# Optimization experiments

Measured on AMD Instinct MI355X. Metric: run time of the kernel, lower is better.

The kernel has to match this reference:

```python
import math
import jax, jax.numpy as jnp
import numpy as np

D_MODEL = 1024
N_HEADS = 16
HEAD_DIM = D_MODEL // N_HEADS
B, S = 4, 1024


def setup_inputs() -> dict:
    key = jax.random.key(0)
    ks = jax.random.split(key, 20)
    def lin(kw, kb):
        # torch nn.Linear: weight [out, in], y = x @ W.T + b
        w = jax.random.normal(kw, (D_MODEL, D_MODEL), jnp.float32) * 0.02
        b = jax.random.normal(kb, (D_MODEL,), jnp.float32) * 0.02
        return w, b
    inp = {
        'global_feat': jax.random.normal(ks[0], (B, S, D_MODEL), jnp.float32),
        'local_feat': jax.random.normal(ks[1], (B, S, D_MODEL), jnp.float32),
        'text_feat': jax.random.normal(ks[2], (B, S, D_MODEL), jnp.float32),
    }
    names = ['glb_q', 'glb_k', 'glb_v', 'plb_q', 'plb_k', 'plb_v', 'dense']
    for i, n in enumerate(names):
        w, b = lin(ks[3 + 2 * i], ks[4 + 2 * i])
        inp[n + '_w'] = w
        inp[n + '_b'] = b
    return inp


def _heads(x):
    # [B,S,D] -> [B,H,S,dh]
    b, s, _ = x.shape
    return x.reshape(b, s, N_HEADS, HEAD_DIM).transpose(0, 2, 1, 3)


def _merge(x):
    # [B,H,S,dh] -> [B,S,D]
    b, h, s, d = x.shape
    return x.transpose(0, 2, 1, 3).reshape(b, s, h * d)


def reference(global_feat, local_feat, text_feat,
              glb_q_w, glb_q_b, glb_k_w, glb_k_b, glb_v_w, glb_v_b,
              plb_q_w, plb_q_b, plb_k_w, plb_k_b, plb_v_w, plb_v_b,
              dense_w, dense_b):
    scale = 1.0 / math.sqrt(HEAD_DIM)
    gq = _heads(global_feat @ glb_q_w.T + glb_q_b)
    gk = _heads(local_feat @ glb_k_w.T + glb_k_b)
    gv = _heads(local_feat @ glb_v_w.T + glb_v_b)
    pq = _heads(local_feat @ plb_q_w.T + plb_q_b)
    pk = _heads(text_feat @ plb_k_w.T + plb_k_b)
    pv = _heads(text_feat @ plb_v_w.T + plb_v_b)

    glb_probs = jax.nn.softmax(jnp.einsum('bhqd,bhkd->bhqk', gq, gk) * scale, axis=-1)
    plb_probs = jax.nn.softmax(jnp.einsum('bhqd,bhkd->bhqk', pq, pk) * scale, axis=-1)

    # bridge: matmul of the two probability matrices (dropout disabled / eval)
    plb_enhanced = jnp.einsum('bhql,bhlt->bhqt', glb_probs, plb_probs)

    glb_ctx = jnp.einsum('bhqk,bhkd->bhqd', glb_probs, gv)
    plb_ctx = jnp.einsum('bhqt,bhtd->bhqd', plb_enhanced, pv)

    last = _merge(glb_ctx) + _merge(plb_ctx)
    return last @ dense_w.T + dense_b
```

## Files before the change

kernel.cpp:

```cpp
#include <hip/hip_runtime.h>


#define DEVI static __device__ __forceinline__

typedef __attribute__((ext_vector_type(4))) float f32x4;
typedef __attribute__((ext_vector_type(8))) __bf16 bf16x8;
typedef __attribute__((ext_vector_type(8))) short s16x8;
typedef __attribute__((ext_vector_type(4))) short s16x4;

constexpr int S = 1024, D = 1024, NH = 16, DH = 64, NB = 4;
constexpr int M = NB * S;
constexpr int KD = 1024;
constexpr int ND = 1024;
constexpr float QSCALE = 0.18033688011112042f;

DEVI short f2bf(float f) {
  unsigned u = __builtin_bit_cast(unsigned, f);
  u += 0x7FFFu + ((u >> 16) & 1u);
  return (short)(u >> 16);
}

DEVI f32x4 mfma_bf16(s16x8 a, s16x8 b, f32x4 c) {
  return __builtin_amdgcn_mfma_f32_16x16x32_bf16(
      __builtin_bit_cast(bf16x8, a), __builtin_bit_cast(bf16x8, b), c, 0, 0, 0);
}

DEVI void gll16(const void* g, void* l) {
  __builtin_amdgcn_global_load_lds(
      (const __attribute__((address_space(1))) unsigned*)g,
      (__attribute__((address_space(3))) unsigned*)l, 16, 0, 0);
}

struct Ptrs3 { const float* p0; const float* p1; const float* p2; };
struct Ptrs7 { const float* p[7]; };

__global__ __launch_bounds__(256) void cast_inputs(Ptrs3 in, short* __restrict__ out) {
  int b = blockIdx.x;
  int which = b >> 12;
  const float* src = which == 0 ? in.p0 : (which == 1 ? in.p1 : in.p2);
  size_t local = ((size_t)(b & 4095) * 256 + threadIdx.x) * 4;
  f32x4 v = *(const f32x4*)(src + local);
  s16x4 o = { f2bf(v[0]), f2bf(v[1]), f2bf(v[2]), f2bf(v[3]) };
  *(s16x4*)(out + (size_t)which * ((size_t)M * KD) + local) = o;
}

__global__ __launch_bounds__(256) void cast_weights(Ptrs7 in, short* __restrict__ out) {
  int b = blockIdx.x;
  int which = b >> 10;
  size_t local = ((size_t)(b & 1023) * 256 + threadIdx.x) * 4;
  f32x4 v = *(const f32x4*)(in.p[which] + local);
  s16x4 o = { f2bf(v[0]), f2bf(v[1]), f2bf(v[2]), f2bf(v[3]) };
  *(s16x4*)(out + (size_t)which * 1048576 + local) = o;
}

DEVI void stage_ab(const short* A, const short* Bw, int rowBase, int colBase, int k0,
                   short* Asb, short* Bsb, int tid) {
  const int cr = tid >> 2;
  const int cb = (tid & 3) * 16;
  const int sw = ((cr >> 1) & 3) << 4;
  gll16((const char*)(A + (size_t)(rowBase + cr) * KD + k0) + (cb ^ sw), Asb + tid * 8);
  gll16((const char*)(A + (size_t)(rowBase + 64 + cr) * KD + k0) + (cb ^ sw), Asb + (tid + 256) * 8);
  gll16((const char*)(Bw + (size_t)(colBase + cr) * KD + k0) + (cb ^ sw), Bsb + tid * 8);
  gll16((const char*)(Bw + (size_t)(colBase + 64 + cr) * KD + k0) + (cb ^ sw), Bsb + (tid + 256) * 8);
}

struct GemmBatch {
  const short* A[6];
  const float* bias[6];
  void* out[6];
};

__global__ __launch_bounds__(256) void gemm_proj(GemmBatch gb, const short* __restrict__ W) {
  __shared__ short As[2][128 * 32];
  __shared__ short Bs[2][128 * 32];
  const int wg = (blockIdx.x & 7) * 192 + (blockIdx.x >> 3);
  const int z = wg >> 8;
  const int rem = wg & 255;
  const int rowBase = (rem >> 3) * 128, colBase = (rem & 7) * 128;

  const short* A = gb.A[z];
  const short* Bw = W + (size_t)z * ((size_t)KD * ND);
  const float* bias = gb.bias[z];
  const float scale = (z == 0 || z == 3) ? QSCALE : 1.0f;
  const int f32out = (z == 2);

  const int tid = threadIdx.x;
  const int lane = tid & 63, wave = tid >> 6;
  const int wr = wave >> 1, wc = wave & 1;
  const int l15 = lane & 15, lg = lane >> 4;
  const int rs = ((l15 >> 1) & 3) << 3;

  stage_ab(A, Bw, rowBase, colBase, 0, As[0], Bs[0], tid);
  __syncthreads();

  f32x4 acc[4][4] = {};
  int buf = 0;
  for (int k0 = 0; k0 < KD; k0 += 32) {
    if (k0 + 32 < KD)
      stage_ab(A, Bw, rowBase, colBase, k0 + 32, As[buf ^ 1], Bs[buf ^ 1], tid);
    s16x8 af[4], bf[4];
#pragma unroll
    for (int m = 0; m < 4; m++)
      af[m] = *(const s16x8*)(As[buf] + (wr * 64 + m * 16 + l15) * 32 + ((lg * 8) ^ rs));
#pragma unroll
    for (int n = 0; n < 4; n++)
      bf[n] = *(const s16x8*)(Bs[buf] + (wc * 64 + n * 16 + l15) * 32 + ((lg * 8) ^ rs));
#pragma unroll
    for (int m = 0; m < 4; m++)
#pragma unroll
      for (int n = 0; n < 4; n++)
        acc[m][n] = mfma_bf16(af[m], bf[n], acc[m][n]);
    __syncthreads();
    buf ^= 1;
  }

  const int r0 = lg * 4;
#pragma unroll
  for (int m = 0; m < 4; m++)
#pragma unroll
    for (int n = 0; n < 4; n++)
#pragma unroll
      for (int i = 0; i < 4; i++) {
        int row = rowBase + wr * 64 + m * 16 + r0 + i;
        int col = colBase + wc * 64 + n * 16 + l15;
        float v = (acc[m][n][i] + bias[col]) * scale;
        size_t idx = (((size_t)(row >> 10) * NH + (col >> 6)) * S + (row & (S - 1))) * DH + (col & (DH - 1));
        if (f32out) ((float*)gb.out[z])[idx] = v;
        else        ((short*)gb.out[z])[idx] = f2bf(v);
      }
}

__global__ __launch_bounds__(256) void gemm_dense(const short* __restrict__ A,
                                                  const short* __restrict__ Bw,
                                                  const float* __restrict__ bias,
                                                  float* __restrict__ outp) {
  __shared__ short As[2][128 * 32];
  __shared__ short Bs[2][128 * 32];
  const int wg = (blockIdx.x & 7) * 32 + (blockIdx.x >> 3);
  const int rowBase = (wg >> 3) * 128, colBase = (wg & 7) * 128;

  const int tid = threadIdx.x;
  const int lane = tid & 63, wave = tid >> 6;
  const int wr = wave >> 1, wc = wave & 1;
  const int l15 = lane & 15, lg = lane >> 4;
  const int rs = ((l15 >> 1) & 3) << 3;

  stage_ab(A, Bw, rowBase, colBase, 0, As[0], Bs[0], tid);
  __syncthreads();

  f32x4 acc[4][4] = {};
  int buf = 0;
  for (int k0 = 0; k0 < KD; k0 += 32) {
    if (k0 + 32 < KD)
      stage_ab(A, Bw, rowBase, colBase, k0 + 32, As[buf ^ 1], Bs[buf ^ 1], tid);
    s16x8 af[4], bf[4];
#pragma unroll
    for (int m = 0; m < 4; m++)
      af[m] = *(const s16x8*)(As[buf] + (wr * 64 + m * 16 + l15) * 32 + ((lg * 8) ^ rs));
#pragma unroll
    for (int n = 0; n < 4; n++)
      bf[n] = *(const s16x8*)(Bs[buf] + (wc * 64 + n * 16 + l15) * 32 + ((lg * 8) ^ rs));
#pragma unroll
    for (int m = 0; m < 4; m++)
#pragma unroll
      for (int n = 0; n < 4; n++)
        acc[m][n] = mfma_bf16(af[m], bf[n], acc[m][n]);
    __syncthreads();
    buf ^= 1;
  }

  const int r0 = lg * 4;
#pragma unroll
  for (int m = 0; m < 4; m++)
#pragma unroll
    for (int n = 0; n < 4; n++)
#pragma unroll
      for (int i = 0; i < 4; i++) {
        int row = rowBase + wr * 64 + m * 16 + r0 + i;
        int col = colBase + wc * 64 + n * 16 + l15;
        outp[(size_t)row * ND + col] = acc[m][n][i] + bias[col];
      }
}

__global__ __launch_bounds__(256) void transpose_bf16(const short* __restrict__ in,
                                                      short* __restrict__ out) {
  __shared__ short t[64 * 65];
  const int bh = blockIdx.y, s0 = blockIdx.x * 64;
  const int tid = threadIdx.x;
#pragma unroll
  for (int j = 0; j < 16; j++) {
    int e = j * 256 + tid;
    int s = e >> 6, d = e & 63;
    t[d * 65 + s] = in[((size_t)bh * S + s0 + s) * DH + d];
  }
  __syncthreads();
#pragma unroll
  for (int j = 0; j < 16; j++) {
    int e = j * 256 + tid;
    int d = e >> 6, s = e & 63;
    out[((size_t)bh * DH + d) * S + s0 + s] = t[d * 65 + s];
  }
}

__global__ __launch_bounds__(256) void vprime_t(const float* __restrict__ gv,
                                                const float* __restrict__ pa,
                                                short* __restrict__ out) {
  __shared__ short t[64 * 65];
  const int bh = blockIdx.y, s0 = blockIdx.x * 64;
  const int tid = threadIdx.x;
#pragma unroll
  for (int j = 0; j < 16; j++) {
    int e = j * 256 + tid;
    int s = e >> 6, d = e & 63;
    size_t idx = ((size_t)bh * S + s0 + s) * DH + d;
    t[d * 65 + s] = f2bf(gv[idx] + pa[idx]);
  }
  __syncthreads();
#pragma unroll
  for (int j = 0; j < 16; j++) {
    int e = j * 256 + tid;
    int d = e >> 6, s = e & 63;
    out[((size_t)bh * DH + d) * S + s0 + s] = t[d * 65 + s];
  }
}

DEVI void stage_kv(const short* kb, const short* vb, int kt,
                   short* KT, short* VTs, int tid) {
  const int r0 = tid >> 3, cb = (tid & 7) * 16;
  const int r1 = r0 + 32;
  const int sw0 = (r0 & 7) << 4;
  gll16((const char*)kb + (size_t)(kt + r0) * 128 + (cb ^ sw0), KT + tid * 8);
  gll16((const char*)kb + (size_t)(kt + r1) * 128 + (cb ^ sw0), KT + (tid + 256) * 8);
  gll16((const char*)vb + (size_t)r0 * 2048 + (size_t)kt * 2 + (cb ^ sw0), VTs + tid * 8);
  gll16((const char*)vb + (size_t)r1 * 2048 + (size_t)kt * 2 + (cb ^ sw0), VTs + (tid + 256) * 8);
}

template <int OUTMODE>
__global__ __launch_bounds__(256, 4) void attn64(const short* __restrict__ Q,
                                                 const short* __restrict__ Km,
                                                 const short* __restrict__ Vt,
                                                 void* __restrict__ outp) {
  __shared__ short KT[2][64 * 64];
  __shared__ short VTs[2][64 * 64];
  __shared__ short Pl[4][1024];
  const int tid = threadIdx.x, lane = tid & 63, wave = tid >> 6;
  const int l15 = lane & 15, lg = lane >> 4;
  const int w = blockIdx.x;
  const int sw = (w & 7) * 128 + (w >> 3);
  const int bh = sw >> 4;
  const int q0 = (sw & 15) * 64 + wave * 16;

  const short* qp = Q + ((size_t)bh * S + q0 + l15) * DH + lg * 8;
  s16x8 qf0 = *(const s16x8*)qp;
  s16x8 qf1 = *(const s16x8*)(qp + 32);

  const short* kb = Km + (size_t)bh * S * DH;
  const short* vb = Vt + (size_t)bh * DH * S;
  short* myP = Pl[wave];
  const int rsz = (l15 & 7) << 3;
  const s16x8 ones = { 0x3F80, 0x3F80, 0x3F80, 0x3F80, 0x3F80, 0x3F80, 0x3F80, 0x3F80 };

  stage_kv(kb, vb, 0, KT[0], VTs[0], tid);
  __syncthreads();

  f32x4 acc[4] = {};
  f32x4 accS = {};

  for (int kt = 0; kt < S; kt += 64) {
    const int cur = (kt >> 6) & 1;
    if (kt + 64 < S) stage_kv(kb, vb, kt + 64, KT[cur ^ 1], VTs[cur ^ 1], tid);

    f32x4 sf[4];
#pragma unroll
    for (int n = 0; n < 4; n++) {
      const short* kr = KT[cur] + (n * 16 + l15) * 64;
      s16x8 k0 = *(const s16x8*)(kr + ((lg * 8) ^ rsz));
      s16x8 k1 = *(const s16x8*)(kr + ((32 + lg * 8) ^ rsz));
      sf[n] = mfma_bf16(qf0, k0, f32x4{});
      sf[n] = mfma_bf16(qf1, k1, sf[n]);
    }

    f32x4 p[4];
#pragma unroll
    for (int n = 0; n < 4; n++)
#pragma unroll
      for (int i = 0; i < 4; i++) p[n][i] = exp2f(sf[n][i]);

#pragma unroll
    for (int n = 0; n < 4; n++)
#pragma unroll
      for (int i = 0; i < 4; i++) {
        int row = lg * 4 + i;
        myP[row * 64 + ((n * 16 + l15) ^ ((row & 7) << 3))] = f2bf(p[n][i]);
      }
    asm volatile("s_waitcnt lgkmcnt(0)" ::: "memory");
    s16x8 pa0 = *(const s16x8*)(myP + l15 * 64 + ((lg * 8) ^ rsz));
    s16x8 pa1 = *(const s16x8*)(myP + l15 * 64 + ((32 + lg * 8) ^ rsz));

    accS = mfma_bf16(pa0, ones, accS);
    accS = mfma_bf16(pa1, ones, accS);

#pragma unroll
    for (int n = 0; n < 4; n++) {
      const short* vr = VTs[cur] + (n * 16 + l15) * 64;
      s16x8 v0 = *(const s16x8*)(vr + ((lg * 8) ^ rsz));
      s16x8 v1 = *(const s16x8*)(vr + ((32 + lg * 8) ^ rsz));
      acc[n] = mfma_bf16(pa0, v0, acc[n]);
      acc[n] = mfma_bf16(pa1, v1, acc[n]);
    }

    __syncthreads();
  }

  float inv[4];
#pragma unroll
  for (int i = 0; i < 4; i++) inv[i] = 1.f / accS[i];
#pragma unroll
  for (int n = 0; n < 4; n++)
#pragma unroll
    for (int i = 0; i < 4; i++) {
      int qq = q0 + lg * 4 + i;
      int dc = n * 16 + l15;
      float v = acc[n][i] * inv[i];
      if (OUTMODE == 0)
        ((float*)outp)[((size_t)bh * S + qq) * DH + dc] = v;
      else
        ((short*)outp)[((size_t)(bh >> 4) * S + qq) * D + (bh & 15) * DH + dc] = f2bf(v);
    }
}

extern "C" void kernel_launch(void* const* d_in, const int* in_sizes, int n_in,
                              void* d_out, int out_size, void* d_ws, size_t ws_size,
                              hipStream_t stream) {
  const float* xg = (const float*)d_in[0];
  const float* xl = (const float*)d_in[1];
  const float* xt = (const float*)d_in[2];
  const float* wf[7]; const float* bf_[7];
  for (int i = 0; i < 7; i++) { wf[i] = (const float*)d_in[3 + 2 * i]; bf_[i] = (const float*)d_in[4 + 2 * i]; }

  char* ws = (char*)d_ws;
  size_t off = 0;
  auto alloc = [&](size_t bytes) { void* p = ws + off; off += (bytes + 255) & ~(size_t)255; return p; };
  short* x16   = (short*)alloc((size_t)3 * M * KD * 2);
  short* w16   = (short*)alloc((size_t)7 * KD * ND * 2);
  short* gq16  = (short*)alloc((size_t)M * D * 2);
  short* gk16  = (short*)alloc((size_t)M * D * 2);
  float* gv32  = (float*)alloc((size_t)M * D * 4);
  short* pq16  = (short*)alloc((size_t)M * D * 2);
  short* pk16  = (short*)alloc((size_t)M * D * 2);
  short* pv16  = (short*)alloc((size_t)M * D * 2);
  short* pvt16 = (short*)alloc((size_t)M * D * 2);
  float* plb32 = (float*)alloc((size_t)M * D * 4);
  short* vpt16 = (short*)alloc((size_t)M * D * 2);
  short* last16= (short*)alloc((size_t)M * D * 2);
  (void)ws_size; (void)in_sizes; (void)n_in; (void)out_size;

  short* xg16 = x16;
  short* xl16 = x16 + (size_t)M * KD;
  short* xt16 = x16 + (size_t)2 * M * KD;

  Ptrs3 p3{xg, xl, xt};
  cast_inputs<<<3 * 4096, 256, 0, stream>>>(p3, x16);
  Ptrs7 p7; for (int i = 0; i < 7; i++) p7.p[i] = wf[i];
  cast_weights<<<7 * 1024, 256, 0, stream>>>(p7, w16);

  GemmBatch gb;
  gb.A[0] = xg16; gb.A[1] = xl16; gb.A[2] = xl16; gb.A[3] = xl16; gb.A[4] = xt16; gb.A[5] = xt16;
  for (int i = 0; i < 6; i++) gb.bias[i] = bf_[i];
  gb.out[0] = gq16; gb.out[1] = gk16; gb.out[2] = gv32;
  gb.out[3] = pq16; gb.out[4] = pk16; gb.out[5] = pv16;
  gemm_proj<<<1536, 256, 0, stream>>>(gb, w16);

  dim3 gt(S / 64, NB * NH);
  transpose_bf16<<<gt, 256, 0, stream>>>(pv16, pvt16);
  attn64<0><<<1024, 256, 0, stream>>>(pq16, pk16, pvt16, plb32);
  vprime_t<<<gt, 256, 0, stream>>>(gv32, plb32, vpt16);
  attn64<1><<<1024, 256, 0, stream>>>(gq16, gk16, vpt16, last16);

  gemm_dense<<<256, 256, 0, stream>>>(last16, w16 + (size_t)6 * 1048576, bf_[6], (float*)d_out);
}
```

Baseline: 326.1 us.

## Fuse V-prime add/transpose into attention epilogue and widen attention to 128 queries

The first attention kernel now adds the bf16 global V projection in its epilogue and writes the transposed bf16 V' directly, which removes the vprime_t kernel and the fp32 plb/gv intermediates. The gv projection is stored as bf16 instead of fp32, and each wave now handles 32 query rows (128 per block), so every K/V tile staged in LDS is reused across twice as many queries. s_setprio and sched_barrier hints are added around the MFMA sections. In exchange, gv carries bf16 rounding error, register use goes up, the block count halves and occupancy drops to 2 blocks per SM, and the transposed epilogue stores are strided.

```diff
diff --git a/kernel.cpp b/kernel.cpp
--- a/kernel.cpp
+++ b/kernel.cpp
@@ -29,6 +29,11 @@
   __builtin_amdgcn_global_load_lds(
       (const __attribute__((address_space(1))) unsigned*)g,
       (__attribute__((address_space(3))) unsigned*)l, 16, 0, 0);
+}
+
+DEVI float bf2f(short s) {
+  unsigned u = (unsigned)(unsigned short)s << 16;
+  return __builtin_bit_cast(float, u);
 }
 
 struct Ptrs3 { const float* p0; const float* p1; const float* p2; };
@@ -67,7 +72,7 @@
 struct GemmBatch {
   const short* A[6];
   const float* bias[6];
-  void* out[6];
+  short* out[6];
 };
 
 __global__ __launch_bounds__(256) void gemm_proj(GemmBatch gb, const short* __restrict__ W) {
@@ -82,7 +87,6 @@
   const short* Bw = W + (size_t)z * ((size_t)KD * ND);
   const float* bias = gb.bias[z];
   const float scale = (z == 0 || z == 3) ? QSCALE : 1.0f;
-  const int f32out = (z == 2);
 
   const int tid = threadIdx.x;
   const int lane = tid & 63, wave = tid >> 6;
@@ -125,8 +129,7 @@
         int col = colBase + wc * 64 + n * 16 + l15;
         float v = (acc[m][n][i] + bias[col]) * scale;
         size_t idx = (((size_t)(row >> 10) * NH + (col >> 6)) * S + (row & (S - 1))) * DH + (col & (DH - 1));
-        if (f32out) ((float*)gb.out[z])[idx] = v;
-        else        ((short*)gb.out[z])[idx] = f2bf(v);
+        gb.out[z][idx] = f2bf(v);
       }
 }
 
@@ -192,28 +195,6 @@
     int e = j * 256 + tid;
     int s = e >> 6, d = e & 63;
     t[d * 65 + s] = in[((size_t)bh * S + s0 + s) * DH + d];
-  }
-  __syncthreads();
-#pragma unroll
-  for (int j = 0; j < 16; j++) {
-    int e = j * 256 + tid;
-    int d = e >> 6, s = e & 63;
-    out[((size_t)bh * DH + d) * S + s0 + s] = t[d * 65 + s];
-  }
-}
-
-__global__ __launch_bounds__(256) void vprime_t(const float* __restrict__ gv,
-                                                const float* __restrict__ pa,
-                                                short* __restrict__ out) {
-  __shared__ short t[64 * 65];
-  const int bh = blockIdx.y, s0 = blockIdx.x * 64;
-  const int tid = threadIdx.x;
-#pragma unroll
-  for (int j = 0; j < 16; j++) {
-    int e = j * 256 + tid;
-    int s = e >> 6, d = e & 63;
-    size_t idx = ((size_t)bh * S + s0 + s) * DH + d;
-    t[d * 65 + s] = f2bf(gv[idx] + pa[idx]);
   }
   __syncthreads();
 #pragma unroll
@@ -236,23 +217,28 @@
 }
 
 template <int OUTMODE>
-__global__ __launch_bounds__(256, 4) void attn64(const short* __restrict__ Q,
-                                                 const short* __restrict__ Km,
-                                                 const short* __restrict__ Vt,
-                                                 void* __restrict__ outp) {
+__global__ __launch_bounds__(256, 2) void attn128(const short* __restrict__ Q,
+                                                  const short* __restrict__ Km,
+                                                  const short* __restrict__ Vt,
+                                                  const short* __restrict__ gv,
+                                                  void* __restrict__ outp) {
   __shared__ short KT[2][64 * 64];
   __shared__ short VTs[2][64 * 64];
-  __shared__ short Pl[4][1024];
+  __shared__ short Pl[4][32 * 64];
   const int tid = threadIdx.x, lane = tid & 63, wave = tid >> 6;
   const int l15 = lane & 15, lg = lane >> 4;
   const int w = blockIdx.x;
-  const int sw = (w & 7) * 128 + (w >> 3);
-  const int bh = sw >> 4;
-  const int q0 = (sw & 15) * 64 + wave * 16;
-
-  const short* qp = Q + ((size_t)bh * S + q0 + l15) * DH + lg * 8;
-  s16x8 qf0 = *(const s16x8*)qp;
-  s16x8 qf1 = *(const s16x8*)(qp + 32);
+  const int sw = (w & 7) * 64 + (w >> 3);
+  const int bh = sw >> 3;
+  const int q0 = (sw & 7) * 128 + wave * 32;
+
+  s16x8 qf[2][2];
+#pragma unroll
+  for (int q = 0; q < 2; q++) {
+    const short* qp = Q + ((size_t)bh * S + q0 + q * 16 + l15) * DH + lg * 8;
+    qf[q][0] = *(const s16x8*)qp;
+    qf[q][1] = *(const s16x8*)(qp + 32);
+  }
 
   const short* kb = Km + (size_t)bh * S * DH;
   const short* vb = Vt + (size_t)bh * DH * S;
@@ -263,70 +249,102 @@
   stage_kv(kb, vb, 0, KT[0], VTs[0], tid);
   __syncthreads();
 
-  f32x4 acc[4] = {};
-  f32x4 accS = {};
+  f32x4 acc[2][4] = {};
+  f32x4 accS[2] = {};
 
   for (int kt = 0; kt < S; kt += 64) {
     const int cur = (kt >> 6) & 1;
     if (kt + 64 < S) stage_kv(kb, vb, kt + 64, KT[cur ^ 1], VTs[cur ^ 1], tid);
 
-    f32x4 sf[4];
+    f32x4 sf[2][4];
+    __builtin_amdgcn_s_setprio(1);
 #pragma unroll
     for (int n = 0; n < 4; n++) {
       const short* kr = KT[cur] + (n * 16 + l15) * 64;
       s16x8 k0 = *(const s16x8*)(kr + ((lg * 8) ^ rsz));
       s16x8 k1 = *(const s16x8*)(kr + ((32 + lg * 8) ^ rsz));
-      sf[n] = mfma_bf16(qf0, k0, f32x4{});
-      sf[n] = mfma_bf16(qf1, k1, sf[n]);
-    }
-
-    f32x4 p[4];
-#pragma unroll
-    for (int n = 0; n < 4; n++)
-#pragma unroll
-      for (int i = 0; i < 4; i++) p[n][i] = exp2f(sf[n][i]);
-
-#pragma unroll
-    for (int n = 0; n < 4; n++)
-#pragma unroll
-      for (int i = 0; i < 4; i++) {
-        int row = lg * 4 + i;
-        myP[row * 64 + ((n * 16 + l15) ^ ((row & 7) << 3))] = f2bf(p[n][i]);
-      }
+#pragma unroll
+      for (int q = 0; q < 2; q++) {
+        sf[q][n] = mfma_bf16(qf[q][0], k0, f32x4{});
+        sf[q][n] = mfma_bf16(qf[q][1], k1, sf[q][n]);
+      }
+    }
+    __builtin_amdgcn_s_setprio(0);
+
+#pragma unroll
+    for (int q = 0; q < 2; q++)
+#pragma unroll
+      for (int n = 0; n < 4; n++)
+#pragma unroll
+        for (int i = 0; i < 4; i++) sf[q][n][i] = exp2f(sf[q][n][i]);
+
+#pragma unroll
+    for (int q = 0; q < 2; q++)
+#pragma unroll
+      for (int n = 0; n < 4; n++)
+#pragma unroll
+        for (int i = 0; i < 4; i++) {
+          int row = q * 16 + lg * 4 + i;
+          myP[row * 64 + ((n * 16 + l15) ^ ((row & 7) << 3))] = f2bf(sf[q][n][i]);
+        }
     asm volatile("s_waitcnt lgkmcnt(0)" ::: "memory");
-    s16x8 pa0 = *(const s16x8*)(myP + l15 * 64 + ((lg * 8) ^ rsz));
-    s16x8 pa1 = *(const s16x8*)(myP + l15 * 64 + ((32 + lg * 8) ^ rsz));
-
-    accS = mfma_bf16(pa0, ones, accS);
-    accS = mfma_bf16(pa1, ones, accS);
-
+    __builtin_amdgcn_sched_barrier(0);
+    s16x8 pa[2][2];
+#pragma unroll
+    for (int q = 0; q < 2; q++) {
+      pa[q][0] = *(const s16x8*)(myP + (q * 16 + l15) * 64 + ((lg * 8) ^ rsz));
+      pa[q][1] = *(const s16x8*)(myP + (q * 16 + l15) * 64 + ((32 + lg * 8) ^ rsz));
+    }
+
+    __builtin_amdgcn_s_setprio(1);
+#pragma unroll
+    for (int q = 0; q < 2; q++) {
+      accS[q] = mfma_bf16(pa[q][0], ones, accS[q]);
+      accS[q] = mfma_bf16(pa[q][1], ones, accS[q]);
+    }
 #pragma unroll
     for (int n = 0; n < 4; n++) {
       const short* vr = VTs[cur] + (n * 16 + l15) * 64;
       s16x8 v0 = *(const s16x8*)(vr + ((lg * 8) ^ rsz));
       s16x8 v1 = *(const s16x8*)(vr + ((32 + lg * 8) ^ rsz));
-      acc[n] = mfma_bf16(pa0, v0, acc[n]);
-      acc[n] = mfma_bf16(pa1, v1, acc[n]);
-    }
+#pragma unroll
+      for (int q = 0; q < 2; q++) {
+        acc[q][n] = mfma_bf16(pa[q][0], v0, acc[q][n]);
+        acc[q][n] = mfma_bf16(pa[q][1], v1, acc[q][n]);
+      }
+    }
+    __builtin_amdgcn_s_setprio(0);
 
     __syncthreads();
   }
 
-  float inv[4];
-#pragma unroll
-  for (int i = 0; i < 4; i++) inv[i] = 1.f / accS[i];
-#pragma unroll
-  for (int n = 0; n < 4; n++)
-#pragma unroll
-    for (int i = 0; i < 4; i++) {
-      int qq = q0 + lg * 4 + i;
-      int dc = n * 16 + l15;
-      float v = acc[n][i] * inv[i];
-      if (OUTMODE == 0)
-        ((float*)outp)[((size_t)bh * S + qq) * DH + dc] = v;
-      else
-        ((short*)outp)[((size_t)(bh >> 4) * S + qq) * D + (bh & 15) * DH + dc] = f2bf(v);
-    }
+#pragma unroll
+  for (int q = 0; q < 2; q++) {
+    float inv[4];
+#pragma unroll
+    for (int i = 0; i < 4; i++) inv[i] = 1.f / accS[q][i];
+#pragma unroll
+    for (int n = 0; n < 4; n++) {
+      const int dc = n * 16 + l15;
+      if (OUTMODE == 0) {
+        const int qq0 = q0 + q * 16 + lg * 4;
+        s16x4 o;
+#pragma unroll
+        for (int i = 0; i < 4; i++) {
+          float g = bf2f(gv[((size_t)bh * S + qq0 + i) * DH + dc]);
+          o[i] = f2bf(acc[q][n][i] * inv[i] + g);
+        }
+        *(s16x4*)((short*)outp + ((size_t)bh * DH + dc) * S + qq0) = o;
+      } else {
+#pragma unroll
+        for (int i = 0; i < 4; i++) {
+          int qq = q0 + q * 16 + lg * 4 + i;
+          ((short*)outp)[((size_t)(bh >> 4) * S + qq) * D + (bh & 15) * DH + dc] =
+              f2bf(acc[q][n][i] * inv[i]);
+        }
+      }
+    }
+  }
 }
 
 extern "C" void kernel_launch(void* const* d_in, const int* in_sizes, int n_in,
@@ -345,12 +363,11 @@
   short* w16   = (short*)alloc((size_t)7 * KD * ND * 2);
   short* gq16  = (short*)alloc((size_t)M * D * 2);
   short* gk16  = (short*)alloc((size_t)M * D * 2);
-  float* gv32  = (float*)alloc((size_t)M * D * 4);
+  short* gv16  = (short*)alloc((size_t)M * D * 2);
   short* pq16  = (short*)alloc((size_t)M * D * 2);
   short* pk16  = (short*)alloc((size_t)M * D * 2);
   short* pv16  = (short*)alloc((size_t)M * D * 2);
   short* pvt16 = (short*)alloc((size_t)M * D * 2);
-  float* plb32 = (float*)alloc((size_t)M * D * 4);
   short* vpt16 = (short*)alloc((size_t)M * D * 2);
   short* last16= (short*)alloc((size_t)M * D * 2);
   (void)ws_size; (void)in_sizes; (void)n_in; (void)out_size;
@@ -367,15 +384,14 @@
   GemmBatch gb;
   gb.A[0] = xg16; gb.A[1] = xl16; gb.A[2] = xl16; gb.A[3] = xl16; gb.A[4] = xt16; gb.A[5] = xt16;
   for (int i = 0; i < 6; i++) gb.bias[i] = bf_[i];
-  gb.out[0] = gq16; gb.out[1] = gk16; gb.out[2] = gv32;
+  gb.out[0] = gq16; gb.out[1] = gk16; gb.out[2] = gv16;
   gb.out[3] = pq16; gb.out[4] = pk16; gb.out[5] = pv16;
   gemm_proj<<<1536, 256, 0, stream>>>(gb, w16);
 
   dim3 gt(S / 64, NB * NH);
   transpose_bf16<<<gt, 256, 0, stream>>>(pv16, pvt16);
-  attn64<0><<<1024, 256, 0, stream>>>(pq16, pk16, pvt16, plb32);
-  vprime_t<<<gt, 256, 0, stream>>>(gv32, plb32, vpt16);
-  attn64<1><<<1024, 256, 0, stream>>>(gq16, gk16, vpt16, last16);
+  attn128<0><<<512, 256, 0, stream>>>(pq16, pk16, pvt16, gv16, vpt16);
+  attn128<1><<<512, 256, 0, stream>>>(gq16, gk16, vpt16, nullptr, last16);
 
   gemm_dense<<<256, 256, 0, stream>>>(last16, w16 + (size_t)6 * 1048576, bf_[6], (float*)d_out);
 }
```

New measurement: 296.9 us. 1.1x faster.
